# Optimization experiments

Hardware: AMD Instinct MI355X
Metric: run time of the kernel (lower is better)

Reference implementation:

```python
import jax, jax.numpy as jnp
import numpy as np
import math

V, D, H, DFF, NL, CTX = 32000, 512, 8, 2048, 2, 1024
B, S = 2, 1024

def ln(x, w, eps=1e-5):
    mu = jnp.mean(x, axis=-1, keepdims=True)
    var = jnp.var(x, axis=-1, keepdims=True)
    return (x - mu) / jnp.sqrt(var + eps) * w

def setup_inputs() -> dict:
    key = jax.random.key(0)
    ks = jax.random.split(key, 10)
    inp = {
        "x": jax.random.randint(ks[0], (B, S), 0, V),
        "wte": jax.random.normal(ks[1], (V, D), jnp.float32) * 0.02,
        "wpe": jax.random.normal(ks[2], (CTX + 1, D), jnp.float32) * 0.02,
        "ln_e_w": jnp.ones((D,), jnp.float32),
        "ln_p_w": jnp.ones((D,), jnp.float32),
        "ln_f_w": jnp.ones((D,), jnp.float32),
        "ln_mlp_w": jnp.ones((D,), jnp.float32),
        "W_q_diag": jax.random.normal(ks[3], (H, D), jnp.float32) * 0.02,
        "W_k_diag": jax.random.normal(ks[4], (H, D), jnp.float32) * 0.02,
        "W_o": jax.random.normal(ks[5], (NL, D, D * H), jnp.float32) * (0.02 / math.sqrt(2 * NL)),
        "mlp_w1": jax.random.normal(ks[6], (DFF, D), jnp.float32) * 0.02,
        "mlp_w2": jax.random.normal(ks[7], (D, DFF), jnp.float32) * 0.02,
    }
    return inp

def reference(x, wte, wpe, ln_e_w, ln_p_w, ln_f_w, ln_mlp_w, W_q_diag, W_k_diag, W_o, mlp_w1, mlp_w2):
    Bsz, Sl = x.shape
    e = ln(wte[x], ln_e_w)                       # (B,S,D)
    p = ln(wpe[: Sl + 1], ln_p_w)                # (S+1,D), identical across batch
    Q = p[1:][None, :, :] * W_q_diag[:, None, :]   # (H,S,D)
    K = p[:-1][None, :, :] * W_k_diag[:, None, :]  # (H,S,D)
    krn = jnp.einsum('hsd,htd->hst', Q, K) / math.sqrt(D)
    mask = jnp.tril(jnp.ones((Sl, Sl), bool))
    krn = jnp.where(mask[None], krn, 0.0)        # (H,S,S)
    wn = 1.0 / (jnp.arange(Sl, dtype=jnp.float32) + 1.0)  # W_N diagonal

    f_k = jnp.zeros_like(e)
    for i in range(NL):
        # R = softmax over S of (V,D)@(B,D,S) -> (B,V,S)
        R = jax.nn.softmax(jnp.einsum('vd,bsd->bvs', wte, f_k), axis=-1)
        ex_wte = jnp.einsum('bvs,vd->bsd', R, wte)
        ex_wte = ex_wte / jnp.sum(R, axis=1)[..., None]  # normalize by sum over V
        Vt = e - ex_wte                                   # (B,S,D)
        delta = jnp.einsum('hst,btd->bhsd', krn, Vt)      # (B,H,S,D)
        delta = delta * wn[None, None, :, None]           # W_N row scaling
        delta = jnp.transpose(delta, (0, 2, 1, 3)).reshape(Bsz, Sl, H * D)
        delta = delta @ W_o[i].T                          # (B,S,D)
        f_k = f_k + delta
        # use_ff MLP block
        h = ln(f_k, ln_mlp_w)
        f_k = f_k + jax.nn.gelu(h @ mlp_w1.T, approximate=False) @ mlp_w2.T

    out = ln(f_k, ln_f_w)
    logits = out[:, -1:, :] @ wte.T               # (B,1,V), targets=None branch
    return logits
```

## Files before the change

### kernel.cpp

```cpp
#include <hip/hip_runtime.h>

#define DV   512
#define SV   1024
#define BV   2
#define VV   32000
#define HV   8
#define DFFV 2048
#define NLV  2
#define KCX  25

typedef __bf16 bf16;
typedef __bf16 bf16x4 __attribute__((ext_vector_type(4)));
typedef __bf16 bf16x8 __attribute__((ext_vector_type(8)));
typedef float  f32x4  __attribute__((ext_vector_type(4)));

__device__ __forceinline__ void lds_dma16(const void* g, void* l) {
  __builtin_amdgcn_global_load_lds(
      (const __attribute__((address_space(1))) unsigned int*)g,
      (__attribute__((address_space(3))) unsigned int*)l,
      16, 0, 0);
}

template<typename OUT>
__device__ __forceinline__ void row_ln_512(const float* __restrict__ src,
                                           const float* __restrict__ w,
                                           OUT* __restrict__ dst, int lane) {
  const float4 a = *(const float4*)(src + lane*8);
  const float4 b = *(const float4*)(src + lane*8 + 4);
  float s = a.x+a.y+a.z+a.w + b.x+b.y+b.z+b.w;
  float q = a.x*a.x+a.y*a.y+a.z*a.z+a.w*a.w + b.x*b.x+b.y*b.y+b.z*b.z+b.w*b.w;
#pragma unroll
  for (int off = 32; off > 0; off >>= 1) {
    s += __shfl_down(s, off, 64);
    q += __shfl_down(q, off, 64);
  }
  s = __shfl(s, 0, 64); q = __shfl(q, 0, 64);
  const float mu   = s * (1.0f/512.0f);
  const float rstd = rsqrtf(q * (1.0f/512.0f) - mu*mu + 1e-5f);
  const float4 wa = *(const float4*)(w + lane*8);
  const float4 wb = *(const float4*)(w + lane*8 + 4);
  OUT* d = dst + lane*8;
  d[0] = (OUT)((a.x-mu)*rstd*wa.x);
  d[1] = (OUT)((a.y-mu)*rstd*wa.y);
  d[2] = (OUT)((a.z-mu)*rstd*wa.z);
  d[3] = (OUT)((a.w-mu)*rstd*wa.w);
  d[4] = (OUT)((b.x-mu)*rstd*wb.x);
  d[5] = (OUT)((b.y-mu)*rstd*wb.y);
  d[6] = (OUT)((b.z-mu)*rstd*wb.z);
  d[7] = (OUT)((b.w-mu)*rstd*wb.w);
}

__global__ void embed_ln_k(const int* __restrict__ x, const float* __restrict__ wte,
                           const float* __restrict__ w, float* __restrict__ e, int nrows) {
  int row = blockIdx.x * 4 + (threadIdx.x >> 6);
  if (row >= nrows) return;
  int tok = x[row];
  row_ln_512<float>(wte + (long)tok * DV, w, e + (long)row * DV, threadIdx.x & 63);
}

__global__ void rows_ln_f32_k(const float* __restrict__ src, const float* __restrict__ w,
                              float* __restrict__ dst, int nrows) {
  int row = blockIdx.x * 4 + (threadIdx.x >> 6);
  if (row >= nrows) return;
  row_ln_512<float>(src + (long)row * DV, w, dst + (long)row * DV, threadIdx.x & 63);
}

__global__ void final_ln_k(const float* __restrict__ f_k, const float* __restrict__ w,
                           float* __restrict__ obuf) {
  int b = threadIdx.x >> 6;
  if (b >= BV) return;
  row_ln_512<float>(f_k + ((long)b * SV + (SV - 1)) * DV, w, obuf + (long)b * DV,
                    threadIdx.x & 63);
}

__global__ void cast_f2b_k(const float* __restrict__ in, bf16* __restrict__ o, long n) {
  long i = ((long)blockIdx.x * 256 + threadIdx.x) * 4;
  if (i >= n) return;
  float4 v = *(const float4*)(in + i);
  o[i+0] = (bf16)v.x; o[i+1] = (bf16)v.y; o[i+2] = (bf16)v.z; o[i+3] = (bf16)v.w;
}

__global__ void wte_prep_k(const float* __restrict__ wte, bf16* __restrict__ wb,
                           bf16* __restrict__ wbT, float* __restrict__ wm) {
  __shared__ float t[32][33];
  __shared__ float cpart[8][32];
  const int d0 = blockIdx.x * 32, v0 = blockIdx.y * 32;
  const int tx = threadIdx.x, ty = threadIdx.y;
  float csum = 0.f;
#pragma unroll
  for (int k = 0; k < 4; k++) {
    const int vl = ty*4 + k;
    const float val = wte[(long)(v0+vl)*DV + d0+tx];
    t[vl][tx] = val;
    csum += val;
  }
  cpart[ty][tx] = csum;
  __syncthreads();
  const int tid = ty*32 + tx;
  const int r = tid >> 3, c = (tid & 7) * 4;
  {
    bf16x4 o;
    o[0] = (bf16)t[r][c];   o[1] = (bf16)t[r][c+1];
    o[2] = (bf16)t[r][c+2]; o[3] = (bf16)t[r][c+3];
    *(bf16x4*)(&wb[(long)(v0+r)*DV + d0+c]) = o;
  }
  {
    bf16x4 o;
    o[0] = (bf16)t[c][r];   o[1] = (bf16)t[c+1][r];
    o[2] = (bf16)t[c+2][r]; o[3] = (bf16)t[c+3][r];
    *(bf16x4*)(&wbT[(long)(d0+r)*VV + v0+c]) = o;
  }
  if (ty == 0) {
    float s = 0.f;
#pragma unroll
    for (int k = 0; k < 8; k++) s += cpart[k][tx];
    atomicAdd(&wm[d0+tx], s);
  }
}

__global__ void qk_prep_k(const float* __restrict__ pn, const float* __restrict__ Wq,
                          const float* __restrict__ Wk, bf16* __restrict__ Qh,
                          bf16* __restrict__ Kh) {
  const int s = blockIdx.x, hh = blockIdx.y;
  const int d = threadIdx.x * 4;
  const float4 q  = *(const float4*)(pn + (long)(s+1)*DV + d);
  const float4 kk = *(const float4*)(pn + (long)s*DV + d);
  const float4 aq = *(const float4*)(Wq + (long)hh*DV + d);
  const float4 ak = *(const float4*)(Wk + (long)hh*DV + d);
  const long o = ((long)hh*SV + s)*DV + d;
  Qh[o+0]=(bf16)(q.x*aq.x);  Qh[o+1]=(bf16)(q.y*aq.y);
  Qh[o+2]=(bf16)(q.z*aq.z);  Qh[o+3]=(bf16)(q.w*aq.w);
  Kh[o+0]=(bf16)(kk.x*ak.x); Kh[o+1]=(bf16)(kk.y*ak.y);
  Kh[o+2]=(bf16)(kk.z*ak.z); Kh[o+3]=(bf16)(kk.w*ak.w);
}

__global__ void colsum_reduce_k(const float* __restrict__ part, float* __restrict__ cs) {
  const int s = blockIdx.x * 256 + threadIdx.x;
  const int b = blockIdx.y;
  const float* pp = part + (long)b * (VV/128) * SV;
  float acc = 0.f;
  for (int v = 0; v < VV/128; v++) acc += pp[(long)v * SV + s];
  cs[(long)b * SV + s] = acc;
}

__global__ void freduce_ln_k(const float* __restrict__ part, float* __restrict__ f_k,
                             const float* __restrict__ w, bf16* __restrict__ hbuf, int KC) {
  const int row = blockIdx.x * 4 + (threadIdx.x >> 6);
  const int lane = threadIdx.x & 63;
  const int b = row >> 10;
  const long ro = (long)row * DV + lane*8;
  const long po = (long)(row & (SV-1)) * DV + lane*8;
  float v[8];
  { const float4 a = *(const float4*)(f_k + ro);
    const float4 c = *(const float4*)(f_k + ro + 4);
    v[0]=a.x;v[1]=a.y;v[2]=a.z;v[3]=a.w;v[4]=c.x;v[5]=c.y;v[6]=c.z;v[7]=c.w; }
  for (int c = 0; c < KC; c++) {
    const float* pp = part + ((long)(b*KC + c))*SV*DV + po;
    const float4 a = *(const float4*)pp;
    const float4 d = *(const float4*)(pp + 4);
    v[0]+=a.x;v[1]+=a.y;v[2]+=a.z;v[3]+=a.w;v[4]+=d.x;v[5]+=d.y;v[6]+=d.z;v[7]+=d.w;
  }
  { float4 o1={v[0],v[1],v[2],v[3]}, o2={v[4],v[5],v[6],v[7]};
    *(float4*)(f_k + ro) = o1; *(float4*)(f_k + ro + 4) = o2; }
  float s = 0.f, q = 0.f;
#pragma unroll
  for (int k = 0; k < 8; k++) { s += v[k]; q += v[k]*v[k]; }
#pragma unroll
  for (int off = 32; off > 0; off >>= 1) {
    s += __shfl_down(s, off, 64);
    q += __shfl_down(q, off, 64);
  }
  s = __shfl(s, 0, 64); q = __shfl(q, 0, 64);
  const float mu   = s * (1.0f/512.0f);
  const float rstd = rsqrtf(q * (1.0f/512.0f) - mu*mu + 1e-5f);
  const float4 wa = *(const float4*)(w + lane*8);
  const float4 wb = *(const float4*)(w + lane*8 + 4);
  bf16* d = hbuf + (long)row * DV + lane*8;
  d[0] = (bf16)((v[0]-mu)*rstd*wa.x);
  d[1] = (bf16)((v[1]-mu)*rstd*wa.y);
  d[2] = (bf16)((v[2]-mu)*rstd*wa.z);
  d[3] = (bf16)((v[3]-mu)*rstd*wa.w);
  d[4] = (bf16)((v[4]-mu)*rstd*wb.x);
  d[5] = (bf16)((v[5]-mu)*rstd*wb.y);
  d[6] = (bf16)((v[6]-mu)*rstd*wb.z);
  d[7] = (bf16)((v[7]-mu)*rstd*wb.w);
}

__global__ void freduce_cast_k(const float* __restrict__ part, float* __restrict__ f_k,
                               bf16* __restrict__ fb, int KC, int do_cast) {
  const long i = ((long)blockIdx.x * 256 + threadIdx.x) * 4;
  const int  b = (int)(i / ((long)SV*DV));
  const long r = i % ((long)SV*DV);
  float4 acc = *(const float4*)(f_k + i);
  for (int c = 0; c < KC; c++) {
    const float4 v = *(const float4*)(part + ((long)(b*KC + c))*SV*DV + r);
    acc.x += v.x; acc.y += v.y; acc.z += v.z; acc.w += v.w;
  }
  *(float4*)(f_k + i) = acc;
  if (do_cast) {
    bf16x4 o; o[0]=(bf16)acc.x; o[1]=(bf16)acc.y; o[2]=(bf16)acc.z; o[3]=(bf16)acc.w;
    *(bf16x4*)(&fb[i]) = o;
  }
}

__global__ void vt_part_k(const float* __restrict__ e, const bf16* __restrict__ pb,
                          const float* __restrict__ cs, bf16* __restrict__ VtT) {
  __shared__ float t[32][33];
  const int d0 = blockIdx.x * 32, s0 = blockIdx.y * 32;
  const int tx = threadIdx.x, ty = threadIdx.y;
#pragma unroll
  for (int k = 0; k < 4; k++) {
    const int sl = ty + k*8;
    const long off = (long)(s0+sl)*DV + d0+tx;
    float acc = 0.f;
    for (int c = 0; c < KCX; c++) acc += (float)pb[(long)c*SV*DV + off];
    t[sl][tx] = e[off] - acc / cs[s0 + sl];
  }
  __syncthreads();
#pragma unroll
  for (int k = 0; k < 4; k++) {
    const int dl = ty + k*8;
    VtT[(long)(d0+dl)*SV + s0+tx] = (bf16)t[tx][dl];
  }
}

__global__ void vt0_transpose_k(const float* __restrict__ e, const float* __restrict__ wm,
                                bf16* __restrict__ VtT) {
  __shared__ float t[32][33];
  const int d0 = blockIdx.x * 32, s0 = blockIdx.y * 32;
  const int tx = threadIdx.x, ty = threadIdx.y;
  const float mval = wm[d0 + tx] * (1.0f / (float)VV);
#pragma unroll
  for (int k = 0; k < 4; k++) {
    const int sl = ty + k*8;
    t[sl][tx] = e[(long)(s0+sl)*DV + d0+tx] - mval;
  }
  __syncthreads();
#pragma unroll
  for (int k = 0; k < 4; k++) {
    const int dl = ty + k*8;
    VtT[(long)(d0+dl)*SV + s0+tx] = (bf16)t[tx][dl];
  }
}

__global__ void logits_k(const float* __restrict__ obuf, const float* __restrict__ wte,
                         float* __restrict__ out, int V) {
  const int wv = threadIdx.x >> 6, lane = threadIdx.x & 63;
  const int v = blockIdx.x * 4 + wv;
  const float* wr = wte + (long)v * DV;
  const float4 a  = *(const float4*)(wr + lane*8);
  const float4 c  = *(const float4*)(wr + lane*8 + 4);
  const float4 oa0 = *(const float4*)(obuf + lane*8);
  const float4 ob0 = *(const float4*)(obuf + lane*8 + 4);
  const float4 oa1 = *(const float4*)(obuf + DV + lane*8);
  const float4 ob1 = *(const float4*)(obuf + DV + lane*8 + 4);
  float d0 = a.x*oa0.x + a.y*oa0.y + a.z*oa0.z + a.w*oa0.w
           + c.x*ob0.x + c.y*ob0.y + c.z*ob0.z + c.w*ob0.w;
  float d1 = a.x*oa1.x + a.y*oa1.y + a.z*oa1.z + a.w*oa1.w
           + c.x*ob1.x + c.y*ob1.y + c.z*ob1.z + c.w*ob1.w;
#pragma unroll
  for (int off = 32; off > 0; off >>= 1) {
    d0 += __shfl_down(d0, off, 64);
    d1 += __shfl_down(d1, off, 64);
  }
  if (lane == 0) { out[v] = d0; out[(long)V + v] = d1; }
}

__device__ __forceinline__ long xcd_swz(long lin, long nwg) {
  const long qq = nwg >> 3, rr = nwg & 7;
  const long xcd = lin & 7, idx = lin >> 3;
  return (xcd < rr ? xcd * (qq + 1) : rr * (qq + 1) + (xcd - rr) * qq) + idx;
}

struct GemmArgs {
  const bf16* A; const bf16* B;
  float* Cf; bf16* Cb;
  int K, lda, ldb, ldc;
  long sAh, sAb, sBh, sBb, sCh, sCb;
  int Hmod, KC, causal, swap;
  float scale;
};

template<int EPI>
__global__ __launch_bounds__(256)
void gemm_nt(GemmArgs g) {
  __shared__ bf16 As[2][128*32];
  __shared__ bf16 Bs[2][128*32];
  const int tid = threadIdx.x;
  int bx = blockIdx.x, by = blockIdx.y, z = blockIdx.z;
  {
    const int nbx = gridDim.x, nby = gridDim.y;
    const long nwg = (long)nbx * nby * gridDim.z;
    long lin = xcd_swz(bx + (long)nbx * (by + (long)nby * z), nwg);
    bx = (int)(lin % nbx);
    const long t2 = lin / nbx;
    by = (int)(t2 % nby);
    z  = (int)(t2 / nby);
  }
  const int chunk = z % g.KC;
  const int zo = z / g.KC;
  const int h = zo % g.Hmod;
  const int b = zo / g.Hmod;
  if (g.swap) { int t = bx; bx = by; by = t; }
  const int m0 = by * 128;
  const int n0 = bx * 128;
  const long coff = (long)h * g.sCh + (long)b * g.sCb;

  if (EPI == 3 && n0 > m0 + 127) return;

  const bf16* A = g.A + (long)h * g.sAh + (long)b * g.sAb;
  const bf16* B = g.B + (long)h * g.sBh + (long)b * g.sBb;
  const int lane = tid & 63;
  const int wv = tid >> 6;
  const int wm = (wv >> 1) * 64;
  const int wn = (wv & 1) * 64;
  const int frow = lane & 15;
  const int quad = lane >> 4;
  const int sg8  = ((lane & 3) ^ ((lane >> 3) & 3)) * 8;
  const int drow = lane >> 2;

  const f32x4 fzero = {0.f, 0.f, 0.f, 0.f};
  f32x4 acc[4][4];
#pragma unroll
  for (int i = 0; i < 4; i++)
#pragma unroll
    for (int j = 0; j < 4; j++) acc[i][j] = fzero;

  int k0, klen;
  if (g.causal) { k0 = 0; klen = min(g.K, m0 + 128); }
  else          { klen = g.K / g.KC; k0 = chunk * klen; }

  auto stage = [&](int buf, int kk) {
#pragma unroll
    for (int c = 0; c < 2; c++) {
      const int rb = c*64 + wv*16;
      lds_dma16(A + (long)(m0 + rb + drow) * g.lda + kk + sg8, &As[buf][rb*32]);
      lds_dma16(B + (long)(n0 + rb + drow) * g.ldb + kk + sg8, &Bs[buf][rb*32]);
    }
  };

  const int nsteps = klen >> 5;
  int cur = 0;
  stage(0, k0);
  for (int it = 0; it < nsteps; ++it) {
    if (it + 1 < nsteps) {
      stage(cur ^ 1, k0 + (it + 1) * 32);
      asm volatile("s_waitcnt vmcnt(4)" ::: "memory");
    } else {
      asm volatile("s_waitcnt vmcnt(0)" ::: "memory");
    }
    __builtin_amdgcn_s_barrier();
    bf16x8 af[4], bfr[4];
    const int sw = (frow >> 1) & 3;
#pragma unroll
    for (int i = 0; i < 4; i++)
      af[i] = *(const bf16x8*)(&As[cur][(wm + i*16 + frow)*32 + ((quad ^ sw))*8]);
#pragma unroll
    for (int j = 0; j < 4; j++)
      bfr[j] = *(const bf16x8*)(&Bs[cur][(wn + j*16 + frow)*32 + ((quad ^ sw))*8]);
#pragma unroll
    for (int i = 0; i < 4; i++)
#pragma unroll
      for (int j = 0; j < 4; j++)
        acc[i][j] = __builtin_amdgcn_mfma_f32_16x16x32_bf16(af[i], bfr[j], acc[i][j], 0, 0, 0);
    __builtin_amdgcn_s_barrier();
    cur ^= 1;
  }

  const int rb = quad * 4;
#pragma unroll
  for (int i = 0; i < 4; i++) {
#pragma unroll
    for (int j = 0; j < 4; j++) {
#pragma unroll
      for (int r = 0; r < 4; r++) {
        const int gm = m0 + wm + i*16 + rb + r;
        const int gn = n0 + wn + j*16 + frow;
        const float v = acc[i][j][r];
        if (EPI == 2) {
          g.Cb[coff + (long)gm * g.ldc + gn] = (bf16)v;
        } else if (EPI == 3) {
          const float val = (gn <= gm) ? v * g.scale / (float)(gm + 1) : 0.0f;
          g.Cb[coff + (long)gm * g.ldc + gn] = (bf16)val;
        } else if (EPI == 4) {
          const float ge = 0.5f * v * (1.0f + erff(v * 0.70710678118f));
          g.Cb[coff + (long)gm * g.ldc + gn] = (bf16)ge;
        } else if (EPI == 6) {
          g.Cf[(long)(b*g.KC + chunk) * g.sCh + (long)gm * g.ldc + gn] = v;
        }
      }
    }
  }
}

template<int EPI>
__global__ __launch_bounds__(512)
void gemm256(GemmArgs g) {
  __shared__ bf16 As[2][256*64];
  __shared__ bf16 Bs[2][256*64];
  const int tid = threadIdx.x;
  int bm = blockIdx.x, bn = blockIdx.y, z = blockIdx.z;
  {
    const int nbx = gridDim.x, nby = gridDim.y;
    const long nwg = (long)nbx * nby * gridDim.z;
    long lin = xcd_swz(bm + (long)nbx * (bn + (long)nby * z), nwg);
    bm = (int)(lin % nbx);
    const long t2 = lin / nbx;
    bn = (int)(t2 % nby);
    z  = (int)(t2 / nby);
  }
  const int b = z / g.KC, chunk = z % g.KC;
  const int m0 = bm * 256, n0 = bn * 256;
  const bf16* A = g.A + (long)b * g.sAb;
  const int lane = tid & 63, wv = tid >> 6;
  const int wm = (wv >> 2) * 128, wn = (wv & 3) * 64;
  const int frow = lane & 15, quad = lane >> 4;
  const int sg8  = ((lane & 7) ^ (lane >> 3)) * 8;
  const int drow = lane >> 3;

  const f32x4 fzero = {0.f, 0.f, 0.f, 0.f};
  f32x4 acc[8][4];
#pragma unroll
  for (int i = 0; i < 8; i++)
#pragma unroll
    for (int j = 0; j < 4; j++) acc[i][j] = fzero;

  const int klen = g.K / g.KC;
  const int k0 = chunk * klen;

  auto stage = [&](int buf, int kk) {
#pragma unroll
    for (int c = 0; c < 4; c++) {
      const int rb = c*64 + wv*8;
      lds_dma16(A   + (long)(m0 + rb + drow) * g.lda + kk + sg8, &As[buf][rb*64]);
      lds_dma16(g.B + (long)(n0 + rb + drow) * g.ldb + kk + sg8, &Bs[buf][rb*64]);
    }
  };

  const int nsteps = klen >> 6;
  int cur = 0;
  stage(0, k0);
  for (int it = 0; it < nsteps; ++it) {
    if (it + 1 < nsteps) {
      stage(cur ^ 1, k0 + (it + 1) * 64);
      asm volatile("s_waitcnt vmcnt(8)" ::: "memory");
    } else {
      asm volatile("s_waitcnt vmcnt(0)" ::: "memory");
    }
    __builtin_amdgcn_s_barrier();
    const int sw = frow & 7;
#pragma unroll
    for (int ks = 0; ks < 2; ks++) {
      bf16x8 af[8], bfr[4];
#pragma unroll
      for (int j = 0; j < 4; j++)
        bfr[j] = *(const bf16x8*)(&Bs[cur][(wn + j*16 + frow)*64 + (((ks*4 + quad) ^ sw))*8]);
#pragma unroll
      for (int i = 0; i < 8; i++)
        af[i] = *(const bf16x8*)(&As[cur][(wm + i*16 + frow)*64 + (((ks*4 + quad) ^ sw))*8]);
#pragma unroll
      for (int i = 0; i < 8; i++)
#pragma unroll
        for (int j = 0; j < 4; j++)
          acc[i][j] = __builtin_amdgcn_mfma_f32_16x16x32_bf16(af[i], bfr[j], acc[i][j], 0, 0, 0);
    }
    __builtin_amdgcn_s_barrier();
    cur ^= 1;
  }

  const int rb4 = quad * 4;
  if (EPI == 5) {
    bf16* Cb = g.Cb + (long)b * g.sCb;
    float* Cf = g.Cf + (long)b * g.sBh;
    const int vblk = (n0 + wn) >> 7;
#pragma unroll
    for (int i = 0; i < 8; i++) {
#pragma unroll
      for (int r = 0; r < 4; r++) {
        const int gm = m0 + wm + i*16 + rb4 + r;
        float rs = 0.f;
#pragma unroll
        for (int j = 0; j < 4; j++) {
          const int gn = n0 + wn + j*16 + frow;
          const float ev = __expf(acc[i][j][r]);
          Cb[(long)gm * g.ldc + gn] = (bf16)ev;
          rs += ev;
        }
#pragma unroll
        for (int off = 1; off < 16; off <<= 1)
          rs += __shfl_xor(rs, off, 64);
        if (frow == 0) atomicAdd(Cf + (long)vblk * SV + gm, rs);
      }
    }
  } else {
#pragma unroll
    for (int i = 0; i < 8; i++) {
#pragma unroll
      for (int j = 0; j < 4; j++) {
#pragma unroll
        for (int r = 0; r < 4; r++) {
          const int gm = m0 + wm + i*16 + rb4 + r;
          const int gn = n0 + wn + j*16 + frow;
          g.Cb[(long)z * g.sCh + (long)gm * g.ldc + gn] = (bf16)acc[i][j][r];
        }
      }
    }
  }
}

static void layer_tail(int il, bf16* krn, bf16* VtT, bf16* U_rs, bf16* Wo_b,
                       float* f_k, bf16* f_k_b, bf16* hbuf, bf16* Gbuf, float* fpart,
                       bf16* w1_b, bf16* w2_b, const float* lnmw, int do_cast,
                       hipStream_t stream) {
  {
    GemmArgs g = {};
    g.A = krn; g.B = VtT; g.Cb = U_rs;
    g.K = SV; g.lda = SV; g.ldb = SV; g.ldc = HV*DV;
    g.sAh = (long)SV*SV; g.sBb = (long)DV*SV;
    g.sCh = DV; g.sCb = (long)SV*HV*DV;
    g.Hmod = HV; g.KC = 1; g.causal = 1;
    gemm_nt<2><<<dim3(DV/128, SV/128, BV*HV), 256, 0, stream>>>(g);
  }
  {
    GemmArgs g = {};
    g.A = U_rs; g.B = Wo_b + (long)il*DV*HV*DV; g.Cf = fpart;
    g.K = HV*DV; g.lda = HV*DV; g.ldb = HV*DV; g.ldc = DV;
    g.sAb = (long)SV*HV*DV; g.sCh = (long)SV*DV;
    g.Hmod = 1; g.KC = 8; g.causal = 0;
    gemm_nt<6><<<dim3(DV/128, SV/128, BV*8), 256, 0, stream>>>(g);
  }
  freduce_ln_k<<<dim3(BV*SV/4), 256, 0, stream>>>(fpart, f_k, lnmw, hbuf, 8);
  {
    GemmArgs g = {};
    g.A = hbuf; g.B = w1_b; g.Cb = Gbuf;
    g.K = DV; g.lda = DV; g.ldb = DV; g.ldc = DFFV;
    g.sAb = (long)SV*DV; g.sCb = (long)SV*DFFV;
    g.Hmod = 1; g.KC = 1; g.causal = 0;
    gemm_nt<4><<<dim3(DFFV/128, SV/128, BV), 256, 0, stream>>>(g);
  }
  {
    GemmArgs g = {};
    g.A = Gbuf; g.B = w2_b; g.Cf = fpart;
    g.K = DFFV; g.lda = DFFV; g.ldb = DFFV; g.ldc = DV;
    g.sAb = (long)SV*DFFV; g.sCh = (long)SV*DV;
    g.Hmod = 1; g.KC = 8; g.causal = 0;
    gemm_nt<6><<<dim3(DV/128, SV/128, BV*8), 256, 0, stream>>>(g);
  }
  freduce_cast_k<<<dim3(BV*SV*DV/4/256), 256, 0, stream>>>(fpart, f_k, f_k_b, 8, do_cast);
}

extern "C" void kernel_launch(void* const* d_in, const int* in_sizes, int n_in,
                              void* d_out, int out_size, void* d_ws, size_t ws_size,
                              hipStream_t stream) {
  const int*   x    = (const int*)d_in[0];
  const float* wte  = (const float*)d_in[1];
  const float* wpe  = (const float*)d_in[2];
  const float* lnew = (const float*)d_in[3];
  const float* lnpw = (const float*)d_in[4];
  const float* lnfw = (const float*)d_in[5];
  const float* lnmw = (const float*)d_in[6];
  const float* Wq   = (const float*)d_in[7];
  const float* Wk   = (const float*)d_in[8];
  const float* Wo   = (const float*)d_in[9];
  const float* w1   = (const float*)d_in[10];
  const float* w2   = (const float*)d_in[11];
  float* out = (float*)d_out;
  (void)in_sizes; (void)n_in; (void)out_size;

  char* p = (char*)d_ws;
  auto alloc = [&](size_t bytes) -> void* {
    void* r = (void*)p;
    p += (bytes + 255) & ~(size_t)255;
    return r;
  };
  float* e      = (float*)alloc((size_t)BV*SV*DV*4);
  float* pn     = (float*)alloc((size_t)(SV+1)*DV*4);
  bf16*  wteT_b = (bf16*)alloc((size_t)DV*VV*2);
  bf16*  wte_b  = (bf16*)alloc((size_t)VV*DV*2);
  bf16*  krn    = (bf16*)alloc((size_t)HV*SV*SV*2);
  bf16*  Wo_b   = (bf16*)alloc((size_t)NLV*DV*HV*DV*2);
  bf16*  w1_b   = (bf16*)alloc((size_t)DFFV*DV*2);
  bf16*  w2_b   = (bf16*)alloc((size_t)DV*DFFV*2);
  float* f_k    = (float*)alloc((size_t)BV*SV*DV*4);
  bf16*  f_k_b  = (bf16*)alloc((size_t)BV*SV*DV*2);
  bf16*  expart = (bf16*)alloc((size_t)KCX*SV*DV*2);
  bf16*  VtT    = (bf16*)alloc((size_t)BV*DV*SV*2);
  bf16*  hbuf   = (bf16*)alloc((size_t)BV*SV*DV*2);
  float* colsum = (float*)alloc((size_t)BV*SV*4);
  float* part   = (float*)alloc((size_t)BV*(VV/128)*SV*4);
  float* obuf   = (float*)alloc((size_t)BV*DV*4);
  float* wmean  = (float*)alloc((size_t)DV*4);
  char*  arena  = (char*)alloc((size_t)SV*VV*2);
  bf16*  Qh     = (bf16*)arena;
  bf16*  Kh     = (bf16*)(arena + (size_t)HV*SV*DV*2);
  bf16*  PT     = (bf16*)arena;
  bf16*  U_rs   = (bf16*)arena;
  bf16*  Gbuf   = (bf16*)(arena + (size_t)BV*SV*HV*DV*2);
  float* fpart  = (float*)(arena + (size_t)BV*SV*HV*DV*2 + (size_t)BV*SV*DFFV*2);
  char*  psave  = p;
  bf16*  PT2    = (bf16*)alloc((size_t)BV*SV*VV*2);
  bf16*  expart2= (bf16*)alloc((size_t)BV*KCX*SV*DV*2);
  const int batched = ((size_t)(p - (char*)d_ws) <= ws_size);
  if (!batched) p = psave;

  hipMemsetAsync(f_k,   0, (size_t)BV*SV*DV*4, stream);
  hipMemsetAsync(f_k_b, 0, (size_t)BV*SV*DV*2, stream);
  hipMemsetAsync(wmean, 0, (size_t)DV*4, stream);
  wte_prep_k<<<dim3(DV/32, VV/32), dim3(32,8), 0, stream>>>(wte, wte_b, wteT_b, wmean);
  cast_f2b_k<<<dim3((NLV*DV*HV*DV/4+255)/256), 256, 0, stream>>>(Wo, Wo_b, (long)NLV*DV*HV*DV);
  cast_f2b_k<<<dim3((DFFV*DV/4+255)/256), 256, 0, stream>>>(w1, w1_b, (long)DFFV*DV);
  cast_f2b_k<<<dim3((DV*DFFV/4+255)/256), 256, 0, stream>>>(w2, w2_b, (long)DV*DFFV);
  embed_ln_k<<<dim3(BV*SV/4), 256, 0, stream>>>(x, wte, lnew, e, BV*SV);
  rows_ln_f32_k<<<dim3((SV+1+3)/4), 256, 0, stream>>>(wpe, lnpw, pn, SV+1);
  qk_prep_k<<<dim3(SV, HV), 128, 0, stream>>>(pn, Wq, Wk, Qh, Kh);

  {
    GemmArgs g = {};
    g.A = Qh; g.B = Kh; g.Cb = krn;
    g.K = DV; g.lda = DV; g.ldb = DV; g.ldc = SV;
    g.sAh = (long)SV*DV; g.sBh = (long)SV*DV; g.sCh = (long)SV*SV;
    g.Hmod = HV; g.KC = 1; g.causal = 0;
    g.scale = 0.044194173824159216f;
    gemm_nt<3><<<dim3(SV/128, SV/128, HV), 256, 0, stream>>>(g);
  }

  for (int b = 0; b < BV; b++)
    vt0_transpose_k<<<dim3(DV/32, SV/32), dim3(32,8), 0, stream>>>(
        e + (long)b*SV*DV, wmean, VtT + (long)b*DV*SV);
  layer_tail(0, krn, VtT, U_rs, Wo_b, f_k, f_k_b, hbuf, Gbuf, fpart,
             w1_b, w2_b, lnmw, 1, stream);

  hipMemsetAsync(part, 0, (size_t)BV*(VV/128)*SV*4, stream);
  if (batched) {
    {
      GemmArgs g = {};
      g.A = f_k_b; g.B = wte_b; g.Cb = PT2; g.Cf = part;
      g.K = DV; g.lda = DV; g.ldb = DV; g.ldc = VV;
      g.sAb = (long)SV*DV; g.sCb = (long)SV*VV; g.sBh = (long)(VV/128)*SV;
      g.KC = 1;
      gemm256<5><<<dim3(SV/256, VV/256, BV), 512, 0, stream>>>(g);
    }
    colsum_reduce_k<<<dim3(SV/256, BV), 256, 0, stream>>>(part, colsum);
    {
      GemmArgs g = {};
      g.A = PT2; g.B = wteT_b; g.Cb = expart2;
      g.K = VV; g.lda = VV; g.ldb = VV; g.ldc = DV;
      g.sAb = (long)SV*VV; g.sCh = (long)SV*DV;
      g.KC = KCX;
      gemm256<7><<<dim3(SV/256, DV/256, BV*KCX), 512, 0, stream>>>(g);
    }
    for (int b = 0; b < BV; b++)
      vt_part_k<<<dim3(DV/32, SV/32), dim3(32,8), 0, stream>>>(
          e + (long)b*SV*DV, expart2 + (long)b*KCX*SV*DV, colsum + (long)b*SV,
          VtT + (long)b*DV*SV);
  } else {
    for (int b = 0; b < BV; b++) {
      {
        GemmArgs g = {};
        g.A = f_k_b + (long)b*SV*DV; g.B = wte_b; g.Cb = PT;
        g.Cf = part + (long)b*(VV/128)*SV;
        g.K = DV; g.lda = DV; g.ldb = DV; g.ldc = VV;
        g.KC = 1;
        gemm256<5><<<dim3(SV/256, VV/256, 1), 512, 0, stream>>>(g);
      }
      colsum_reduce_k<<<dim3(SV/256, 1), 256, 0, stream>>>(
          part + (long)b*(VV/128)*SV, colsum);
      {
        GemmArgs g = {};
        g.A = PT; g.B = wteT_b; g.Cb = expart;
        g.K = VV; g.lda = VV; g.ldb = VV; g.ldc = DV;
        g.sCh = (long)SV*DV;
        g.KC = KCX;
        gemm256<7><<<dim3(SV/256, DV/256, KCX), 512, 0, stream>>>(g);
      }
      vt_part_k<<<dim3(DV/32, SV/32), dim3(32,8), 0, stream>>>(
          e + (long)b*SV*DV, expart, colsum, VtT + (long)b*DV*SV);
    }
  }
  layer_tail(1, krn, VtT, U_rs, Wo_b, f_k, f_k_b, hbuf, Gbuf, fpart,
             w1_b, w2_b, lnmw, 0, stream);

  final_ln_k<<<1, 256, 0, stream>>>(f_k, lnfw, obuf);
  logits_k<<<dim3(VV/4), 256, 0, stream>>>(obuf, wte, out, VV);
}
```

Before: 528.8 us.

## Use four-stage K=32 LDS pipeline with single barrier in gemm256

Restructures the 256x256 GEMM main loop from a double-buffered K=64 scheme into a four-buffer ring of K=32 slices, prefetching three stages ahead with graded vmcnt waits. The second barrier per iteration goes away because the next stage is issued after the barrier into a buffer that is no longer being read. The LDS swizzle is adapted to 32-wide rows, and MFMA sections are wrapped in s_setprio. The aim is to hide global-load latency better and cut synchronization, in exchange for more loop iterations and a narrower swizzle that may raise LDS bank conflicts.

```diff
diff --git a/kernel.cpp b/kernel.cpp
--- a/kernel.cpp
+++ b/kernel.cpp
@@ -396,8 +396,8 @@
 template<int EPI>
 __global__ __launch_bounds__(512)
 void gemm256(GemmArgs g) {
-  __shared__ bf16 As[2][256*64];
-  __shared__ bf16 Bs[2][256*64];
+  __shared__ bf16 As[4][256*32];
+  __shared__ bf16 Bs[4][256*32];
   const int tid = threadIdx.x;
   int bm = blockIdx.x, bn = blockIdx.y, z = blockIdx.z;
   {
@@ -415,8 +415,8 @@
   const int lane = tid & 63, wv = tid >> 6;
   const int wm = (wv >> 2) * 128, wn = (wv & 3) * 64;
   const int frow = lane & 15, quad = lane >> 4;
-  const int sg8  = ((lane & 7) ^ (lane >> 3)) * 8;
-  const int drow = lane >> 3;
+  const int sg8  = ((lane & 3) ^ ((lane >> 3) & 3)) * 8;
+  const int drow = lane >> 2;
 
   const f32x4 fzero = {0.f, 0.f, 0.f, 0.f};
   f32x4 acc[8][4];
@@ -430,42 +430,39 @@
 
   auto stage = [&](int buf, int kk) {
 #pragma unroll
-    for (int c = 0; c < 4; c++) {
-      const int rb = c*64 + wv*8;
-      lds_dma16(A   + (long)(m0 + rb + drow) * g.lda + kk + sg8, &As[buf][rb*64]);
-      lds_dma16(g.B + (long)(n0 + rb + drow) * g.ldb + kk + sg8, &Bs[buf][rb*64]);
+    for (int c = 0; c < 2; c++) {
+      const int rb = wv*32 + c*16;
+      lds_dma16(A   + (long)(m0 + rb + drow) * g.lda + kk + sg8, &As[buf][rb*32]);
+      lds_dma16(g.B + (long)(n0 + rb + drow) * g.ldb + kk + sg8, &Bs[buf][rb*32]);
     }
   };
 
-  const int nsteps = klen >> 6;
-  int cur = 0;
+  const int nsteps = klen >> 5;
   stage(0, k0);
+  if (nsteps > 1) stage(1, k0 + 32);
+  if (nsteps > 2) stage(2, k0 + 64);
   for (int it = 0; it < nsteps; ++it) {
-    if (it + 1 < nsteps) {
-      stage(cur ^ 1, k0 + (it + 1) * 64);
-      asm volatile("s_waitcnt vmcnt(8)" ::: "memory");
-    } else {
-      asm volatile("s_waitcnt vmcnt(0)" ::: "memory");
-    }
+    if (it + 3 <= nsteps)      asm volatile("s_waitcnt vmcnt(8)" ::: "memory");
+    else if (it + 2 == nsteps) asm volatile("s_waitcnt vmcnt(4)" ::: "memory");
+    else                       asm volatile("s_waitcnt vmcnt(0)" ::: "memory");
     __builtin_amdgcn_s_barrier();
-    const int sw = frow & 7;
-#pragma unroll
-    for (int ks = 0; ks < 2; ks++) {
-      bf16x8 af[8], bfr[4];
+    if (it + 3 < nsteps) stage((it + 3) & 3, k0 + (it + 3) * 32);
+    const int cur = it & 3;
+    const int sl = ((quad ^ ((frow >> 1) & 3))) * 8;
+    bf16x8 af[8], bfr[4];
+#pragma unroll
+    for (int j = 0; j < 4; j++)
+      bfr[j] = *(const bf16x8*)(&Bs[cur][(wn + j*16 + frow)*32 + sl]);
+#pragma unroll
+    for (int i = 0; i < 8; i++)
+      af[i] = *(const bf16x8*)(&As[cur][(wm + i*16 + frow)*32 + sl]);
+    __builtin_amdgcn_s_setprio(1);
+#pragma unroll
+    for (int i = 0; i < 8; i++)
 #pragma unroll
       for (int j = 0; j < 4; j++)
-        bfr[j] = *(const bf16x8*)(&Bs[cur][(wn + j*16 + frow)*64 + (((ks*4 + quad) ^ sw))*8]);
-#pragma unroll
-      for (int i = 0; i < 8; i++)
-        af[i] = *(const bf16x8*)(&As[cur][(wm + i*16 + frow)*64 + (((ks*4 + quad) ^ sw))*8]);
-#pragma unroll
-      for (int i = 0; i < 8; i++)
-#pragma unroll
-        for (int j = 0; j < 4; j++)
-          acc[i][j] = __builtin_amdgcn_mfma_f32_16x16x32_bf16(af[i], bfr[j], acc[i][j], 0, 0, 0);
-    }
-    __builtin_amdgcn_s_barrier();
-    cur ^= 1;
+        acc[i][j] = __builtin_amdgcn_mfma_f32_16x16x32_bf16(af[i], bfr[j], acc[i][j], 0, 0, 0);
+    __builtin_amdgcn_s_setprio(0);
   }
 
   const int rb4 = quad * 4;
```

Measured after the change: 559.2 us. 1.06x slower.
